# Performance work log

Measured on AMD Instinct MI355X. Metric: run time of the kernel, lower is better.

Reference implementation:

```python
import jax, jax.numpy as jnp
import numpy as np

EMBED = 512
HEADS = 8
DIM_HEAD = 64
SCALE = DIM_HEAD ** -0.5


def setup_inputs() -> dict:
    key = jax.random.key(0)
    k1, k2, k3 = jax.random.split(key, 3)
    x = jax.random.normal(k1, (1, EMBED, 64, 64), dtype=jnp.float32)
    # nn.Linear(embed, 3*embed) weight [out, in] -> store transposed [in, out] for x @ W
    W_qkv = jax.random.normal(k2, (EMBED, 3 * EMBED), dtype=jnp.float32) * (EMBED ** -0.5)
    b_qkv = jax.random.normal(k3, (3 * EMBED,), dtype=jnp.float32) * 0.01
    return {"x": x, "W_qkv": W_qkv, "b_qkv": b_qkv}


def reference(x, W_qkv, b_qkv):
    B, E, h, w = x.shape
    N = h * w
    # [B, E, H, W] -> [B, N, E]
    xs = x.reshape(B, E, N).transpose(0, 2, 1)
    qkv = xs @ W_qkv + b_qkv                      # [B, N, 3E]
    q, k, v = jnp.split(qkv, 3, axis=-1)          # each [B, N, E]

    def heads(t):
        return t.reshape(B, N, HEADS, DIM_HEAD).transpose(0, 2, 1, 3)  # [B, H, N, dh]

    q, k, v = heads(q), heads(k), heads(v)
    # raw (non-softmax) attention scores, materialized as in the original
    attn = jnp.einsum('bhqd,bhkd->bhqk', q, k) * SCALE  # [B, H, N, N]
    coarse_attn = attn.sum(axis=-2)                     # sum over queries -> [B, H, N]
    output = jnp.einsum('bhqk,bhkd->bhqd', attn, v)     # [B, H, N, dh]
    return coarse_attn, output
```

## Files before the change

kernel.cpp:

```cpp
#include <hip/hip_runtime.h>


#define N_TOK 4096
#define EMBED 512
#define J3    1536
#define HEADS 8
#define DH    64
#define SCALE 0.125f

typedef float  floatx4  __attribute__((ext_vector_type(4)));
typedef short  shortx8  __attribute__((ext_vector_type(8)));
typedef unsigned short ushortx4 __attribute__((ext_vector_type(4)));
typedef unsigned int u32;
typedef unsigned short ushort;

__device__ inline ushort f2bf(float f) {
    union { float f; u32 u; } x; x.f = f;
    u32 r = x.u + 0x7fffu + ((x.u >> 16) & 1u);
    return (ushort)(r >> 16);
}
__device__ inline float bf2f(ushort u) {
    union { u32 u; float f; } x; x.u = ((u32)u) << 16; return x.f;
}
__device__ static inline void async_copy16(void* lds, const void* g) {
    auto* gp = (const __attribute__((address_space(1))) u32*)g;
    auto* lp = (__attribute__((address_space(3))) u32*)lds;
    __builtin_amdgcn_global_load_lds(gp, lp, 16, 0, 0);
}
__device__ inline int permj(int j) {
    if (j < 512) return j;
    if (j < 1024) return 512 + ((j - 512) >> 6) * 128 + ((j - 512) & 63);
    return 512 + ((j - 1024) >> 6) * 128 + 64 + ((j - 1024) & 63);
}

__global__ __launch_bounds__(256) void prep(const float* __restrict__ x,
                                            const float* __restrict__ W,
                                            ushort* __restrict__ xT,
                                            ushort* __restrict__ WT,
                                            ushort* __restrict__ Wb,
                                            float* __restrict__ xsum) {
    const int t = threadIdx.x;
    int bx = blockIdx.x;
    const bool isx = bx < 64;
    const float* src = isx ? x : W;
    const int C = isx ? N_TOK : J3;
    if (!isx) bx -= 64;
    __shared__ float T[64][65];
    __shared__ float red[256];
    const int c0 = bx * 64, r0 = blockIdx.y * 64;
    #pragma unroll
    for (int k = 0; k < 16; ++k) {
        int i = t + 256 * k; int r = i >> 6, c = i & 63;
        T[r][c] = src[(size_t)(r0 + r) * C + c0 + c];
    }
    __syncthreads();
    if (isx) {
        int row = t >> 2, seg = (t & 3) * 16;
        float s = 0.f;
        #pragma unroll
        for (int cc = 0; cc < 16; ++cc) s += T[row][seg + cc];
        red[t] = s;
    }
    #pragma unroll
    for (int k = 0; k < 4; ++k) {
        int i = t + 256 * k; int cr = i >> 4, cc4 = (i & 15) * 4;
        ushortx4 o = { f2bf(T[cc4 + 0][cr]), f2bf(T[cc4 + 1][cr]),
                       f2bf(T[cc4 + 2][cr]), f2bf(T[cc4 + 3][cr]) };
        int dr = isx ? (c0 + cr) : permj(c0 + cr);
        ushort* dst = isx ? xT : WT;
        *(ushortx4*)&dst[(size_t)dr * 512 + r0 + cc4] = o;
    }
    if (!isx) {
        #pragma unroll
        for (int k = 0; k < 4; ++k) {
            int i = t + 256 * k; int rr = i >> 4, c4 = (i & 15) * 4;
            ushortx4 o = { f2bf(T[rr][c4 + 0]), f2bf(T[rr][c4 + 1]),
                           f2bf(T[rr][c4 + 2]), f2bf(T[rr][c4 + 3]) };
            *(ushortx4*)&Wb[(size_t)(r0 + rr) * J3 + c0 + c4] = o;
        }
    }
    if (isx) {
        __syncthreads();
        if ((t & 3) == 0)
            atomicAdd(&xsum[r0 + (t >> 2)], red[t] + red[t + 1] + red[t + 2] + red[t + 3]);
    }
}

__global__ __launch_bounds__(256) void kvm(const ushort* __restrict__ xT,
                                           const ushort* __restrict__ WT,
                                           const float* __restrict__ bias,
                                           float* __restrict__ Mp) {
    const int h = blockIdx.x, ch = blockIdx.y;
    const int j0 = 512 + h * 128, n0 = ch * 128;
    __shared__ __align__(16) char lds[34816];
    short* As = (short*)lds;
    short* Bs = (short*)(lds + 8192);
    short* Kt = (short*)lds;
    short* Vt = (short*)(lds + 17408);
    const int t = threadIdx.x, lane = t & 63, w = t >> 6;
    const int wm = w & 1, wn = w >> 1;
    const int quad = lane >> 4, mrow = lane & 15;
    floatx4 acc[4][4] = {};
    for (int e0 = 0; e0 < 512; e0 += 32) {
        __syncthreads();
        #pragma unroll
        for (int s = 0; s < 2; ++s) {
            int i = t + 256 * s; int row = i >> 2, q = i & 3;
            async_copy16((char*)As + (size_t)w * 1024 + (size_t)s * 4096,
                         xT + (size_t)(n0 + row) * 512 + e0 + q * 8);
            async_copy16((char*)Bs + (size_t)w * 1024 + (size_t)s * 4096,
                         WT + (size_t)(j0 + row) * 512 + e0 + q * 8);
        }
        __syncthreads();
        shortx8 a[4], b[4];
        #pragma unroll
        for (int mi = 0; mi < 4; ++mi)
            a[mi] = *(const shortx8*)&As[(wm * 64 + mi * 16 + mrow) * 32 + quad * 8];
        #pragma unroll
        for (int ni = 0; ni < 4; ++ni)
            b[ni] = *(const shortx8*)&Bs[(wn * 64 + ni * 16 + mrow) * 32 + quad * 8];
        #pragma unroll
        for (int mi = 0; mi < 4; ++mi)
            #pragma unroll
            for (int ni = 0; ni < 4; ++ni)
                acc[mi][ni] = __builtin_amdgcn_mfma_f32_16x16x32_bf16(a[mi], b[ni], acc[mi][ni], 0, 0, 0);
    }
    __syncthreads();
    {
        short* ldst = (wn == 0) ? Kt : Vt;
        #pragma unroll
        for (int ni = 0; ni < 4; ++ni) {
            int cl = wn * 64 + ni * 16 + mrow;
            float bj = (cl < 64) ? bias[512 + h * 64 + cl] : bias[1024 + h * 64 + cl - 64];
            int dh = ni * 16 + mrow;
            #pragma unroll
            for (int mi = 0; mi < 4; ++mi)
                #pragma unroll
                for (int r = 0; r < 4; ++r) {
                    int tok = wm * 64 + mi * 16 + quad * 4 + r;
                    ldst[dh * 136 + tok] = (short)f2bf(acc[mi][ni][r] + bj);
                }
        }
    }
    __syncthreads();
    const int dpb = (w & 1) * 32, db = (w >> 1) * 32;
    floatx4 m[2][2] = {};
    #pragma unroll
    for (int kt = 0; kt < 4; ++kt) {
        shortx8 ka[2], vb[2];
        #pragma unroll
        for (int fi = 0; fi < 2; ++fi)
            ka[fi] = *(const shortx8*)&Kt[(dpb + fi * 16 + mrow) * 136 + kt * 32 + quad * 8];
        #pragma unroll
        for (int fj = 0; fj < 2; ++fj)
            vb[fj] = *(const shortx8*)&Vt[(db + fj * 16 + mrow) * 136 + kt * 32 + quad * 8];
        #pragma unroll
        for (int fi = 0; fi < 2; ++fi)
            #pragma unroll
            for (int fj = 0; fj < 2; ++fj)
                m[fi][fj] = __builtin_amdgcn_mfma_f32_16x16x32_bf16(ka[fi], vb[fj], m[fi][fj], 0, 0, 0);
    }
    float* mp = Mp + ((size_t)h * 32 + ch) * 4096;
    #pragma unroll
    for (int fi = 0; fi < 2; ++fi)
        #pragma unroll
        for (int fj = 0; fj < 2; ++fj)
            #pragma unroll
            for (int rr = 0; rr < 4; ++rr)
                mp[(dpb + fi * 16 + quad * 4 + rr) * 64 + db + fj * 16 + mrow] = m[fi][fj][rr];
}

__global__ __launch_bounds__(256) void reduce_build(const float* __restrict__ Mp,
                                                    const ushort* __restrict__ WT,
                                                    const ushort* __restrict__ Wb,
                                                    const float* __restrict__ bias,
                                                    const float* __restrict__ xsum,
                                                    ushort* __restrict__ PT,
                                                    float* __restrict__ rbuf) {
    const int h = blockIdx.x, part = blockIdx.y;
    const int t = threadIdx.x;
    const int dv0 = part * 16;
    __shared__ float Msub[64][17];
    __shared__ float red[256];
    __shared__ float Qs[64];
    {
        int dp = t >> 2, g = t & 3;
        floatx4 s = {0.f, 0.f, 0.f, 0.f};
        #pragma unroll 8
        for (int c = 0; c < 32; ++c)
            s += *(const floatx4*)&Mp[((size_t)(h * 32 + c)) * 4096 + dp * 64 + dv0 + g * 4];
        Msub[dp][g * 4 + 0] = s[0]; Msub[dp][g * 4 + 1] = s[1];
        Msub[dp][g * 4 + 2] = s[2]; Msub[dp][g * 4 + 3] = s[3];
    }
    {
        int jl = t >> 2, sg = t & 3;
        const ushort* wrow = WT + (size_t)(h * 64 + jl) * 512 + sg * 128;
        float qa = 0.f;
        #pragma unroll
        for (int g = 0; g < 16; ++g) {
            shortx8 wv = *(const shortx8*)(wrow + g * 8);
            #pragma unroll
            for (int u = 0; u < 8; ++u)
                qa += bf2f((ushort)wv[u]) * xsum[sg * 128 + g * 8 + u];
        }
        red[t] = qa;
    }
    __syncthreads();
    if (t < 64) Qs[t] = 4096.f * bias[h * 64 + t] + red[t * 4] + red[t * 4 + 1] + red[t * 4 + 2] + red[t * 4 + 3];
    {
        const int lane = t & 63, w = t >> 6;
        const int quad = lane >> 4, mrow = lane & 15;
        const int we0 = w * 128;
        floatx4 acc[8] = {};
        #pragma unroll
        for (int ks = 0; ks < 2; ++ks) {
            shortx8 ahi, alo;
            #pragma unroll
            for (int kq = 0; kq < 8; ++kq) {
                int dk = ks * 32 + quad * 8 + kq;
                float v = SCALE * Msub[dk][mrow];
                ushort hi = f2bf(v);
                ahi[kq] = (short)hi;
                alo[kq] = (short)f2bf(v - bf2f(hi));
            }
            #pragma unroll
            for (int ni = 0; ni < 8; ++ni) {
                shortx8 b = *(const shortx8*)(Wb + (size_t)(we0 + ni * 16 + mrow) * J3 + h * 64 + ks * 32 + quad * 8);
                acc[ni] = __builtin_amdgcn_mfma_f32_16x16x32_bf16(ahi, b, acc[ni], 0, 0, 0);
                acc[ni] = __builtin_amdgcn_mfma_f32_16x16x32_bf16(alo, b, acc[ni], 0, 0, 0);
            }
        }
        #pragma unroll
        for (int ni = 0; ni < 8; ++ni)
            #pragma unroll
            for (int rr = 0; rr < 4; ++rr)
                PT[(size_t)(h * 64 + dv0 + quad * 4 + rr) * 512 + we0 + ni * 16 + mrow] = f2bf(acc[ni][rr]);
    }
    if (t < 16) {
        float s = 0.f;
        #pragma unroll
        for (int dk = 0; dk < 64; ++dk) s += bias[h * 64 + dk] * Msub[dk][t];
        rbuf[h * 64 + dv0 + t] = SCALE * s;
    }
    __syncthreads();
    if (part == 0) {
        for (int e = t; e < 512; e += 256) {
            float s = 0.f;
            #pragma unroll
            for (int g = 0; g < 8; ++g) {
                shortx8 wv = *(const shortx8*)(Wb + (size_t)e * J3 + 512 + h * 64 + g * 8);
                #pragma unroll
                for (int u = 0; u < 8; ++u) s += bf2f((ushort)wv[u]) * Qs[g * 8 + u];
            }
            PT[(size_t)(512 + h) * 512 + e] = f2bf(SCALE * s);
        }
        if (t == 0) {
            float s = 0.f;
            #pragma unroll
            for (int dk = 0; dk < 64; ++dk) s += bias[512 + h * 64 + dk] * Qs[dk];
            rbuf[512 + h] = SCALE * s;
        }
    }
    {
        int idx = h * 4 + part;
        #pragma unroll
        for (int z = 0; z < 2; ++z) {
            int row = 520 + idx * 2 + z;
            if (row < 576) {
                PT[(size_t)row * 512 + t] = 0;
                PT[(size_t)row * 512 + 256 + t] = 0;
                if (t == 0) rbuf[row] = 0.f;
            }
        }
    }
}

__global__ __launch_bounds__(256) void outf(const ushort* __restrict__ xT,
                                            const ushort* __restrict__ PT,
                                            const float* __restrict__ rbuf,
                                            float* __restrict__ out) {
    const int c0 = blockIdx.x * 64, n0 = blockIdx.y * 64;
    const int t = threadIdx.x, lane = t & 63, w = t >> 6;
    const int wm = w & 1, wn = w >> 1;
    const int quad = lane >> 4, mrow = lane & 15;
    const ushort* pa0 = xT + (size_t)(n0 + wm * 32 + mrow) * 512 + quad * 8;
    const ushort* pa1 = pa0 + 16 * 512;
    const ushort* pb0 = PT + (size_t)(c0 + wn * 32 + mrow) * 512 + quad * 8;
    const ushort* pb1 = pb0 + 16 * 512;
    floatx4 acc[2][2] = {};
    #pragma unroll 4
    for (int e0 = 0; e0 < 512; e0 += 32) {
        shortx8 a0 = *(const shortx8*)(pa0 + e0);
        shortx8 a1 = *(const shortx8*)(pa1 + e0);
        shortx8 b0 = *(const shortx8*)(pb0 + e0);
        shortx8 b1 = *(const shortx8*)(pb1 + e0);
        acc[0][0] = __builtin_amdgcn_mfma_f32_16x16x32_bf16(a0, b0, acc[0][0], 0, 0, 0);
        acc[0][1] = __builtin_amdgcn_mfma_f32_16x16x32_bf16(a0, b1, acc[0][1], 0, 0, 0);
        acc[1][0] = __builtin_amdgcn_mfma_f32_16x16x32_bf16(a1, b0, acc[1][0], 0, 0, 0);
        acc[1][1] = __builtin_amdgcn_mfma_f32_16x16x32_bf16(a1, b1, acc[1][1], 0, 0, 0);
    }
    #pragma unroll
    for (int ni = 0; ni < 2; ++ni) {
        int c = c0 + wn * 32 + ni * 16 + mrow;
        float rc = rbuf[c];
        #pragma unroll
        for (int mi = 0; mi < 2; ++mi)
            #pragma unroll
            for (int rr = 0; rr < 4; ++rr) {
                int n = n0 + wm * 32 + mi * 16 + quad * 4 + rr;
                float val = acc[mi][ni][rr] + rc;
                if (c < 512)
                    out[32768 + (size_t)(c >> 6) * 262144 + (size_t)n * 64 + (c & 63)] = val;
                else if (c < 520)
                    out[(size_t)(c - 512) * 4096 + n] = val;
            }
    }
}

extern "C" void kernel_launch(void* const* d_in, const int* in_sizes, int n_in,
                              void* d_out, int out_size, void* d_ws, size_t ws_size,
                              hipStream_t stream) {
    const float* x = (const float*)d_in[0];
    const float* W = (const float*)d_in[1];
    const float* b = (const float*)d_in[2];
    float* out = (float*)d_out;

    ushort* xT = (ushort*)d_ws;
    ushort* WT = xT + (size_t)N_TOK * EMBED;
    ushort* Wb = WT + (size_t)J3 * EMBED;
    ushort* PT = Wb + (size_t)EMBED * J3;
    float*  Mp = (float*)(PT + (size_t)576 * 512);
    float* xsum = Mp + (size_t)HEADS * 32 * 4096;
    float* rbuf = xsum + 512;

    prep<<<dim3(88, 8), 256, 0, stream>>>(x, W, xT, WT, Wb, xsum);
    kvm<<<dim3(8, 32), 256, 0, stream>>>(xT, WT, b, Mp);
    reduce_build<<<dim3(8, 4), 256, 0, stream>>>(Mp, WT, Wb, b, xsum, PT, rbuf);
    outf<<<dim3(9, 64), 256, 0, stream>>>(xT, PT, rbuf, out);
}
```

Measured before the change: 122.6 us.

## Stage outf GEMM tiles in LDS via async copies and double N tile

The final output GEMM no longer reads A and B fragments straight from global memory. Each K-step now stages them into shared memory with async 16-byte copies, and the block tile grows from 64x64 to 128x64, with four M-subtiles per wave. The aim is more reuse of each loaded fragment and coalesced global loads. The costs are two barriers per K-step with no double buffering, and the grid shrinks to 288 blocks, which may leave the 256 CUs poorly balanced.

```diff
diff --git a/kernel.cpp b/kernel.cpp
--- a/kernel.cpp
+++ b/kernel.cpp
@@ -279,35 +279,48 @@
                                             const ushort* __restrict__ PT,
                                             const float* __restrict__ rbuf,
                                             float* __restrict__ out) {
-    const int c0 = blockIdx.x * 64, n0 = blockIdx.y * 64;
+    const int c0 = blockIdx.x * 64, n0 = blockIdx.y * 128;
     const int t = threadIdx.x, lane = t & 63, w = t >> 6;
     const int wm = w & 1, wn = w >> 1;
     const int quad = lane >> 4, mrow = lane & 15;
-    const ushort* pa0 = xT + (size_t)(n0 + wm * 32 + mrow) * 512 + quad * 8;
-    const ushort* pa1 = pa0 + 16 * 512;
-    const ushort* pb0 = PT + (size_t)(c0 + wn * 32 + mrow) * 512 + quad * 8;
-    const ushort* pb1 = pb0 + 16 * 512;
-    floatx4 acc[2][2] = {};
-    #pragma unroll 4
+    __shared__ __align__(16) char lds[12288];
+    short* As = (short*)lds;
+    short* Bs = (short*)(lds + 8192);
+    const int rowB = t >> 2, qb = t & 3;
+    floatx4 acc[4][2] = {};
     for (int e0 = 0; e0 < 512; e0 += 32) {
-        shortx8 a0 = *(const shortx8*)(pa0 + e0);
-        shortx8 a1 = *(const shortx8*)(pa1 + e0);
-        shortx8 b0 = *(const shortx8*)(pb0 + e0);
-        shortx8 b1 = *(const shortx8*)(pb1 + e0);
-        acc[0][0] = __builtin_amdgcn_mfma_f32_16x16x32_bf16(a0, b0, acc[0][0], 0, 0, 0);
-        acc[0][1] = __builtin_amdgcn_mfma_f32_16x16x32_bf16(a0, b1, acc[0][1], 0, 0, 0);
-        acc[1][0] = __builtin_amdgcn_mfma_f32_16x16x32_bf16(a1, b0, acc[1][0], 0, 0, 0);
-        acc[1][1] = __builtin_amdgcn_mfma_f32_16x16x32_bf16(a1, b1, acc[1][1], 0, 0, 0);
+        __syncthreads();
+        #pragma unroll
+        for (int s = 0; s < 2; ++s) {
+            int i = t + 256 * s; int row = i >> 2, q = i & 3;
+            async_copy16((char*)As + (size_t)w * 1024 + (size_t)s * 4096,
+                         xT + (size_t)(n0 + row) * 512 + e0 + q * 8);
+        }
+        async_copy16((char*)Bs + (size_t)w * 1024,
+                     PT + (size_t)(c0 + rowB) * 512 + e0 + qb * 8);
+        __syncthreads();
+        shortx8 a[4], b[2];
+        #pragma unroll
+        for (int mi = 0; mi < 4; ++mi)
+            a[mi] = *(const shortx8*)&As[(wm * 64 + mi * 16 + mrow) * 32 + quad * 8];
+        #pragma unroll
+        for (int ni = 0; ni < 2; ++ni)
+            b[ni] = *(const shortx8*)&Bs[(wn * 32 + ni * 16 + mrow) * 32 + quad * 8];
+        #pragma unroll
+        for (int mi = 0; mi < 4; ++mi)
+            #pragma unroll
+            for (int ni = 0; ni < 2; ++ni)
+                acc[mi][ni] = __builtin_amdgcn_mfma_f32_16x16x32_bf16(a[mi], b[ni], acc[mi][ni], 0, 0, 0);
     }
     #pragma unroll
     for (int ni = 0; ni < 2; ++ni) {
         int c = c0 + wn * 32 + ni * 16 + mrow;
         float rc = rbuf[c];
         #pragma unroll
-        for (int mi = 0; mi < 2; ++mi)
+        for (int mi = 0; mi < 4; ++mi)
             #pragma unroll
             for (int rr = 0; rr < 4; ++rr) {
-                int n = n0 + wm * 32 + mi * 16 + quad * 4 + rr;
+                int n = n0 + wm * 64 + mi * 16 + quad * 4 + rr;
                 float val = acc[mi][ni][rr] + rc;
                 if (c < 512)
                     out[32768 + (size_t)(c >> 6) * 262144 + (size_t)n * 64 + (c & 63)] = val;
@@ -336,5 +349,5 @@
     prep<<<dim3(88, 8), 256, 0, stream>>>(x, W, xT, WT, Wb, xsum);
     kvm<<<dim3(8, 32), 256, 0, stream>>>(xT, WT, b, Mp);
     reduce_build<<<dim3(8, 4), 256, 0, stream>>>(Mp, WT, Wb, b, xsum, PT, rbuf);
-    outf<<<dim3(9, 64), 256, 0, stream>>>(xT, PT, rbuf, out);
-}
+    outf<<<dim3(9, 32), 256, 0, stream>>>(xT, PT, rbuf, out);
+}
```

Result: faster. 110.9 us (-9.5%).
